# Kernel tuning notes

Measured on AMD Instinct MI355X. Metric: run time of the kernel, lower is better.

Reference implementation:

```python
import jax, jax.numpy as jnp
import numpy as np

NUM_CLASSES = 80
IOU_THR = 0.5
SCORE_THR = 0.25
MAX_BBOXES = 100
NEG = -1e9  # sentinel for suppressed scores


def setup_inputs() -> dict:
    key = jax.random.key(0)
    ks = jax.random.split(key, 9)
    B = 8
    def head(i, g):
        return (jax.random.uniform(ks[3*i], (B, g, g, 3, 4), dtype=jnp.float32),
                jax.random.uniform(ks[3*i+1], (B, g, g, 3, 1), dtype=jnp.float32),
                jax.random.normal(ks[3*i+2], (B, g, g, 3, NUM_CLASSES), dtype=jnp.float32))
    b20, p20, c20 = head(0, 20)
    b40, p40, c40 = head(1, 40)
    b80, p80, c80 = head(2, 80)
    return {"bbox20": b20, "p20": p20, "c20": c20,
            "bbox40": b40, "p40": p40, "c40": c40,
            "bbox80": b80, "p80": p80, "c80": c80}


def _iou_one_vs_all(box, boxes):
    # box: (4,) [y1,x1,y2,x2]; boxes: (N,4)
    y1, x1, y2, x2 = box[0], box[1], box[2], box[3]
    Y1, X1, Y2, X2 = boxes[:, 0], boxes[:, 1], boxes[:, 2], boxes[:, 3]
    ih = jnp.maximum(jnp.minimum(y2, Y2) - jnp.maximum(y1, Y1), 0.0)
    iw = jnp.maximum(jnp.minimum(x2, X2) - jnp.maximum(x1, X1), 0.0)
    inter = ih * iw
    union = (y2 - y1) * (x2 - x1) + (Y2 - Y1) * (X2 - X1) - inter
    return jnp.where(union > 0, inter / union, 0.0)


def _nms_single(boxes, scores):
    # boxes (N,4), scores (N,) -> greedy class-agnostic NMS, up to MAX_BBOXES
    sc0 = jnp.where(scores > SCORE_THR, scores, NEG)

    def body(sc, _):
        idx = jnp.argmax(sc)
        s = sc[idx]
        valid = s > NEG * 0.5
        box = boxes[idx]
        iou = _iou_one_vs_all(box, boxes)
        sc = jnp.where(iou > IOU_THR, NEG, sc)
        sc = sc.at[idx].set(NEG)
        ob = jnp.where(valid, jnp.clip(box, 0.0, 1.0), 0.0)  # clip_boxes=True default
        os = jnp.where(valid, s, 0.0)
        return sc, (ob, os, valid)

    _, (b, s, v) = jax.lax.scan(body, sc0, None, length=MAX_BBOXES)
    return b, s, jnp.sum(v.astype(jnp.int32))


def _forward(bbox20, p20, c20, bbox40, p40, c40, bbox80, p80, c80):
    B = bbox20.shape[0]
    bbox = jnp.concatenate([x.reshape(B, -1, 4) for x in (bbox20, bbox40, bbox80)], axis=1)
    p = jnp.concatenate([x.reshape(B, -1) for x in (p20, p40, p80)], axis=1)
    c = jnp.concatenate([x.reshape(B, -1, NUM_CLASSES) for x in (c20, c40, c80)], axis=1)
    cls = jnp.argmax(c, axis=-1).astype(jnp.float32)  # (B,N)
    score = p * cls  # quirky score = objectness * class index (faithful to source)
    b, s, valid = jax.vmap(_nms_single)(bbox, score)
    # classes output: scores had a single class dim in the TF op -> class index 0
    pred = jnp.concatenate([b, s[..., None], jnp.zeros_like(s)[..., None]], axis=-1)
    return pred, valid


def reference(bbox20, p20, c20, bbox40, p40, c40, bbox80, p80, c80):
    return _forward(bbox20, p20, c20, bbox40, p40, c40, bbox80, p80, c80)
```

## Files before the change

### kernel.cpp

```cpp
#include <hip/hip_runtime.h>
#include <hip/hip_bf16.h>

#define NUM_CLASSES 80
#define BATCH 8
#define N20 1200
#define N40 4800
#define N80 19200
#define NANCH 25200
#define NEGV  -1000000000.0f
#define SCORE_THR 0.25f
#define CAP 1024
#define RMAX 192
#define PKCAP 512
#define NHBIN 512
#define THR_LIST 64.0f

typedef unsigned long long ull;

__global__ __launch_bounds__(256) void score_kernel(
        const float* __restrict__ p20, const float* __restrict__ c20,
        const float* __restrict__ p40, const float* __restrict__ c40,
        const float* __restrict__ p80, const float* __restrict__ c80,
        float* __restrict__ scores, unsigned* __restrict__ cand_cnt,
        ull* __restrict__ cand_keys) {
    const int t = threadIdx.x;
    const int lane = t & 63;
    const int b = blockIdx.y;
    const int an = blockIdx.x * 256 + t;
    const bool valid_an = (an < NANCH);
    const int n = valid_an ? an : (NANCH - 1);

    const float *cp, *pp;
    if (n < N20) {
        cp = c20 + ((size_t)b * N20 + n) * NUM_CLASSES;
        pp = p20 + (size_t)b * N20 + n;
    } else if (n < N20 + N40) {
        int a = n - N20;
        cp = c40 + ((size_t)b * N40 + a) * NUM_CLASSES;
        pp = p40 + (size_t)b * N40 + a;
    } else {
        int a = n - N20 - N40;
        cp = c80 + ((size_t)b * N80 + a) * NUM_CLASSES;
        pp = p80 + (size_t)b * N80 + a;
    }

    const float4* c4 = (const float4*)cp;
    float p = *pp;
    float4 v[20];
#pragma unroll
    for (int k = 0; k < 20; k++) v[k] = c4[k];
    __builtin_amdgcn_sched_barrier(0);

    float best = -INFINITY;
    int bi = 0;
#pragma unroll
    for (int k = 0; k < 20; k++) {
        int basei = k * 4;
        if (v[k].x > best) { best = v[k].x; bi = basei; }
        if (v[k].y > best) { best = v[k].y; bi = basei + 1; }
        if (v[k].z > best) { best = v[k].z; bi = basei + 2; }
        if (v[k].w > best) { best = v[k].w; bi = basei + 3; }
    }

    float s = __fmul_rn(p, (float)bi);
    float sval = (s > SCORE_THR) ? s : NEGV;
    if (valid_an) scores[(size_t)b * NANCH + an] = sval;

    bool pred = valid_an && (s >= THR_LIST);
    ull mask = __ballot(pred);
    if (mask != 0ull) {
        int leader = (int)(__ffsll(mask) - 1);
        unsigned basep = 0;
        if (lane == leader) basep = atomicAdd(&cand_cnt[b], (unsigned)__popcll(mask));
        basep = __shfl(basep, leader);
        if (pred) {
            unsigned pos = basep + (unsigned)__popcll(mask & ((1ull << lane) - 1));
            if (pos < (unsigned)CAP)
                cand_keys[(size_t)b * CAP + pos] =
                    ((ull)__float_as_uint(s) << 32)
                  | (ull)(0xFFFFFFFFu - (unsigned)an);
        }
    }
}

__device__ __forceinline__ bool iou_gt(const float4 A, float areaA, const float4 Bx, float areaB) {
    float ih = fmaxf(__fsub_rn(fminf(A.z, Bx.z), fmaxf(A.x, Bx.x)), 0.0f);
    float iw = fmaxf(__fsub_rn(fminf(A.w, Bx.w), fmaxf(A.y, Bx.y)), 0.0f);
    float inter = __fmul_rn(ih, iw);
    float uni = __fsub_rn(__fadd_rn(areaA, areaB), inter);
    if (!(uni > 0.0f)) return false;
    return __fdiv_rn(inter, uni) > 0.5f;
}

__device__ __forceinline__ float4 load_box(int b, int n,
        const float* b20, const float* b40, const float* b80) {
    if (n < N20)       return ((const float4*)b20)[(size_t)b * N20 + n];
    if (n < N20 + N40) return ((const float4*)b40)[(size_t)b * N40 + (n - N20)];
    return ((const float4*)b80)[(size_t)b * N80 + (n - N20 - N40)];
}

__device__ __forceinline__ float box_area(const float4 B) {
    return __fmul_rn(__fsub_rn(B.z, B.x), __fsub_rn(B.w, B.y));
}

__global__ __launch_bounds__(1024) void nms_kernel(
        const float* __restrict__ scores_g,
        const unsigned* __restrict__ cand_cnt,
        const ull* __restrict__ cand_keys,
        const float* __restrict__ b20, const float* __restrict__ b40,
        const float* __restrict__ b80, float* __restrict__ out) {
    __shared__ ull skeys[CAP];
    __shared__ ull pk[PKCAP];
    __shared__ unsigned hist[NHBIN];
    __shared__ ull srt_key[RMAX];
    __shared__ int prt[PKCAP][5];
    __shared__ float4 bboxC[4][RMAX + 1];
    __shared__ ull M[RMAX][4];
    __shared__ ull red[1024];
    __shared__ int sh_V, sh_T;
    __shared__ unsigned sh_pcnt;

    const int t = threadIdx.x;
    const int lane = t & 63;
    const int b = blockIdx.x;

    const unsigned cnt_raw = cand_cnt[b];
    const bool use_list = (cnt_raw <= (unsigned)CAP);
    const int cnt = use_list ? (int)cnt_raw : 0;
    const int nR = min(cnt, RMAX);
    const unsigned need = (unsigned)nR;

    ull kmy = 0ull;
    float4 bmy = make_float4(0.f, 0.f, 0.f, 0.f);
    int mybin = 0;
    if (t < cnt) {
        kmy = cand_keys[(size_t)b * CAP + t];
        skeys[t] = kmy;
        bmy = load_box(b, (int)(0xFFFFFFFFu - (unsigned)(kmy & 0xFFFFFFFFull)),
                       b20, b40, b80);
        unsigned sb = (unsigned)(kmy >> 32);
        mybin = min((int)((sb - 0x42800000u) >> 12), NHBIN - 1);
    }
    if (t < NHBIN) hist[t] = 0u;
    if (t == 0) { sh_V = 0; sh_pcnt = 0u; }
    __syncthreads();

    if (t < cnt) atomicAdd(&hist[mybin], 1u);
    __syncthreads();

    if (t < 64) {
        unsigned h[8], sfx[8];
        const int basei = t * 8;
#pragma unroll
        for (int k = 0; k < 8; k++) h[k] = hist[basei + k];
        unsigned run = 0;
#pragma unroll
        for (int k = 7; k >= 0; k--) { run += h[k]; sfx[k] = run; }
        unsigned s = run;
#pragma unroll
        for (int d = 1; d < 64; d <<= 1) {
            unsigned vv = __shfl_down(s, d);
            if (t + d < 64) s += vv;
        }
        const unsigned above = s - run;
        int bestb = -1;
#pragma unroll
        for (int k = 0; k < 8; k++)
            if (sfx[k] + above >= need) bestb = basei + k;
#pragma unroll
        for (int d = 32; d > 0; d >>= 1) {
            int o = __shfl_down(bestb, d);
            if (t + d < 64) bestb = max(bestb, o);
        }
        if (t == 0) sh_T = max(bestb, 0);
    }
    __syncthreads();

    const bool part = (t < cnt) && (mybin >= sh_T);
    unsigned mypos = 0xFFFFFFFFu;
    {
        ull mask = __ballot(part);
        if (mask != 0ull) {
            int leader = (int)(__ffsll(mask) - 1);
            unsigned basep = 0;
            if (lane == leader) basep = atomicAdd(&sh_pcnt, (unsigned)__popcll(mask));
            basep = __shfl(basep, leader);
            if (part) {
                mypos = basep + (unsigned)__popcll(mask & ((1ull << lane) - 1));
                if (mypos < (unsigned)PKCAP) pk[mypos] = kmy;
            }
        }
    }
    __syncthreads();

    const int m = (int)sh_pcnt;
    const bool fastrank = (m <= PKCAP);

    if (fastrank) {
        const int q = t >> 8, u = t & 255;
        const ull kA = (u < m) ? pk[u] : 0ull;
        const ull kB = (u + 256 < m) ? pk[u + 256] : 0ull;
        const int Q = (m + 3) >> 2;
        const int j0 = q * Q, j1 = min(m, j0 + Q);
        int rA = 0, rB = 0;
#pragma unroll 8
        for (int j = j0; j < j1; j++) {
            ull kj = pk[j];
            rA += (kj > kA) ? 1 : 0;
            rB += (kj > kB) ? 1 : 0;
        }
        prt[u][q] = rA;
        if (u + 256 < PKCAP) prt[u + 256][q] = rB;
        __syncthreads();
        if (part && mypos < (unsigned)PKCAP) {
            int r = prt[mypos][0] + prt[mypos][1] + prt[mypos][2] + prt[mypos][3];
            if (r < RMAX) {
                srt_key[r] = kmy;
#pragma unroll
                for (int c = 0; c < 4; c++) bboxC[c][r] = bmy;
            }
        }
        __syncthreads();
    } else {
        const bool hasA = (t < 512) && (t < cnt);
        const bool hasB = (t < 512) && (t + 512 < cnt);
        ull kA = hasA ? skeys[t] : 0ull;
        ull kB = hasB ? skeys[t + 512] : 0ull;
        int rA = 0, rB = 0;
        if (t < 512) {
#pragma unroll 8
            for (int j = 0; j < cnt; j++) {
                ull kj = skeys[j];
                rA += (kj > kA) ? 1 : 0;
                rB += (kj > kB) ? 1 : 0;
            }
        }
        if (hasA && rA < RMAX) srt_key[rA] = kA;
        if (hasB && rB < RMAX) srt_key[rB] = kB;
        __syncthreads();
        if (t < nR) {
            ull k = srt_key[t];
            float4 B = load_box(b, (int)(0xFFFFFFFFu - (unsigned)(k & 0xFFFFFFFFull)),
                                b20, b40, b80);
#pragma unroll
            for (int c = 0; c < 4; c++) bboxC[c][t] = B;
        }
        __syncthreads();
    }

    {
        const int row = t >> 2, cw = t & 3;
        if (row < RMAX) {
            ull w = 0ull;
            if (row < nR && cw < 3 && cw * 64 < row) {
                const float4 B = bboxC[cw][row];
                const float aB = box_area(B);
                const int jmax = min(64, row - cw * 64);
                const float4* src = &bboxC[cw][cw * 64];
                for (int j = 0; j < jmax; j++) {
                    const float4 C = src[j];
                    w |= ((ull)iou_gt(C, box_area(C), B, aB)) << j;
                }
            }
            M[row][cw] = w;
        }
    }
    __syncthreads();

    int v = 0;
    if (t < 64) {
        ull A0 = 0, A1 = 0, A2 = 0;
        for (int rg = 0; rg < 3 && v < 100; rg++) {
            const int rr = rg * 64 + t;
            const bool valid = (rr < nR);
            ull w0 = 0, w1 = 0, w2 = 0;
            if (valid) { w0 = M[rr][0]; w1 = M[rr][1]; w2 = M[rr][2]; }
            const ull mw = (rg == 0) ? w0 : (rg == 1) ? w1 : w2;
            const bool supE = !valid ||
                (((w0 & A0) | (w1 & A1) | (w2 & A2)) != 0ull);
            ull alive = __ballot(!supE);
            while (alive != 0ull && v < 100) {
                int c = (int)(__ffsll(alive) - 1);
                ull supc = __ballot((bool)((mw >> c) & 1ull));
                alive &= ~(supc | (1ull << c));
                if (rg == 0) A0 |= 1ull << c;
                else if (rg == 1) A1 |= 1ull << c;
                else A2 |= 1ull << c;
                if (t == c) {
                    const float4 B = bboxC[0][rr];
                    float* rowp = out + ((size_t)b * 100 + v) * 6;
                    rowp[0] = fminf(fmaxf(B.x, 0.f), 1.f);
                    rowp[1] = fminf(fmaxf(B.y, 0.f), 1.f);
                    rowp[2] = fminf(fmaxf(B.z, 0.f), 1.f);
                    rowp[3] = fminf(fmaxf(B.w, 0.f), 1.f);
                    rowp[4] = __uint_as_float((unsigned)(srt_key[rr] >> 32));
                    rowp[5] = 0.f;
                }
                v++;
            }
        }
        if (t == 0) sh_V = v;
    }
    __syncthreads();

    const bool need_fb = (!use_list) || (sh_V < 100 && cnt > nR);
    if (need_fb) {
        float* scb = (float*)scores_g + (size_t)b * NANCH;
        int v2 = 0;
        for (int k = 0; k < 100; k++) {
            ull bestk = 0ull;
            for (int i = t; i < NANCH; i += 1024) {
                float sv = scb[i];
                unsigned u = __float_as_uint(sv);
                u ^= (u & 0x80000000u) ? 0xFFFFFFFFu : 0x80000000u;
                ull key = ((ull)u << 32) | (ull)(0xFFFFFFFFu - (unsigned)i);
                if (key > bestk) bestk = key;
            }
            red[t] = bestk;
            __syncthreads();
            for (int ss = 512; ss > 0; ss >>= 1) {
                if (t < ss && red[t + ss] > red[t]) red[t] = red[t + ss];
                __syncthreads();
            }
            ull bk = red[0];
            __syncthreads();
            unsigned u = (unsigned)(bk >> 32);
            u ^= (u & 0x80000000u) ? 0x80000000u : 0xFFFFFFFFu;
            float s = __uint_as_float(u);
            int idx = (int)(0xFFFFFFFFu - (unsigned)(bk & 0xFFFFFFFFull));
            if (!(s > NEGV * 0.5f)) break;
            float4 B = load_box(b, idx, b20, b40, b80);
            float aB = box_area(B);
            for (int i = t; i < NANCH; i += 1024) {
                float sv = scb[i];
                if (sv > NEGV * 0.5f) {
                    float4 C = load_box(b, i, b20, b40, b80);
                    if (iou_gt(B, aB, C, box_area(C))) scb[i] = NEGV;
                }
            }
            if (t == 0) {
                scb[idx] = NEGV;
                float* rowp = out + ((size_t)b * 100 + k) * 6;
                rowp[0] = fminf(fmaxf(B.x, 0.f), 1.f);
                rowp[1] = fminf(fmaxf(B.y, 0.f), 1.f);
                rowp[2] = fminf(fmaxf(B.z, 0.f), 1.f);
                rowp[3] = fminf(fmaxf(B.w, 0.f), 1.f);
                rowp[4] = s;
                rowp[5] = 0.f;
            }
            v2++;
            __syncthreads();
        }
        __syncthreads();
        if (t == 0) sh_V = v2;
        __syncthreads();
    }

    const int V = sh_V;
    for (int i = V * 6 + t; i < 600; i += 1024) out[(size_t)b * 600 + i] = 0.f;
    if (t == 0) out[4800 + b] = (float)V;
}

extern "C" void kernel_launch(void* const* d_in, const int* in_sizes, int n_in,
                              void* d_out, int out_size, void* d_ws, size_t ws_size,
                              hipStream_t stream) {
    const float* b20 = (const float*)d_in[0];
    const float* p20 = (const float*)d_in[1];
    const float* c20 = (const float*)d_in[2];
    const float* b40 = (const float*)d_in[3];
    const float* p40 = (const float*)d_in[4];
    const float* c40 = (const float*)d_in[5];
    const float* b80 = (const float*)d_in[6];
    const float* p80 = (const float*)d_in[7];
    const float* c80 = (const float*)d_in[8];

    float*    scores   = (float*)d_ws;
    unsigned* cand_cnt = (unsigned*)((char*)d_ws + 806400);
    ull*      cand_keys = (ull*)((char*)d_ws + 806464);

    hipMemsetAsync(cand_cnt, 0, BATCH * sizeof(unsigned), stream);

    dim3 sgrid((NANCH + 255) / 256, BATCH);
    score_kernel<<<sgrid, 256, 0, stream>>>(
        p20, c20, p40, c40, p80, c80, scores, cand_cnt, cand_keys);

    nms_kernel<<<BATCH, 1024, 0, stream>>>(
        scores, cand_cnt, cand_keys, b20, b40, b80, (float*)d_out);
}
```

Measured before the change: 164.8 us.

## Fuse score and NMS kernels with per-batch completion counters

Merges the scoring kernel and the NMS kernel into a single launch. The last 8 blocks spin on a per-batch done counter until all 99 scoring blocks for their batch finish, which removes one kernel launch boundary. The NMS part is reworked for 256 threads: it uses finer histogram bins, single-pass rank counting with box loads folded in, and a single box copy in shared memory instead of four. The risks are deadlock if the NMS blocks get scheduled before the scoring blocks and occupy the CUs, and slower NMS and fallback phases from using fewer threads.

Result: slower. 199.7 us (+21.2%).

```diff
diff --git a/kernel.cpp b/kernel.cpp
--- a/kernel.cpp
+++ b/kernel.cpp
@@ -12,76 +12,11 @@
 #define CAP 1024
 #define RMAX 192
 #define PKCAP 512
-#define NHBIN 512
+#define NHBIN 1024
 #define THR_LIST 64.0f
+#define NPB 99
 
 typedef unsigned long long ull;
-
-__global__ __launch_bounds__(256) void score_kernel(
-        const float* __restrict__ p20, const float* __restrict__ c20,
-        const float* __restrict__ p40, const float* __restrict__ c40,
-        const float* __restrict__ p80, const float* __restrict__ c80,
-        float* __restrict__ scores, unsigned* __restrict__ cand_cnt,
-        ull* __restrict__ cand_keys) {
-    const int t = threadIdx.x;
-    const int lane = t & 63;
-    const int b = blockIdx.y;
-    const int an = blockIdx.x * 256 + t;
-    const bool valid_an = (an < NANCH);
-    const int n = valid_an ? an : (NANCH - 1);
-
-    const float *cp, *pp;
-    if (n < N20) {
-        cp = c20 + ((size_t)b * N20 + n) * NUM_CLASSES;
-        pp = p20 + (size_t)b * N20 + n;
-    } else if (n < N20 + N40) {
-        int a = n - N20;
-        cp = c40 + ((size_t)b * N40 + a) * NUM_CLASSES;
-        pp = p40 + (size_t)b * N40 + a;
-    } else {
-        int a = n - N20 - N40;
-        cp = c80 + ((size_t)b * N80 + a) * NUM_CLASSES;
-        pp = p80 + (size_t)b * N80 + a;
-    }
-
-    const float4* c4 = (const float4*)cp;
-    float p = *pp;
-    float4 v[20];
-#pragma unroll
-    for (int k = 0; k < 20; k++) v[k] = c4[k];
-    __builtin_amdgcn_sched_barrier(0);
-
-    float best = -INFINITY;
-    int bi = 0;
-#pragma unroll
-    for (int k = 0; k < 20; k++) {
-        int basei = k * 4;
-        if (v[k].x > best) { best = v[k].x; bi = basei; }
-        if (v[k].y > best) { best = v[k].y; bi = basei + 1; }
-        if (v[k].z > best) { best = v[k].z; bi = basei + 2; }
-        if (v[k].w > best) { best = v[k].w; bi = basei + 3; }
-    }
-
-    float s = __fmul_rn(p, (float)bi);
-    float sval = (s > SCORE_THR) ? s : NEGV;
-    if (valid_an) scores[(size_t)b * NANCH + an] = sval;
-
-    bool pred = valid_an && (s >= THR_LIST);
-    ull mask = __ballot(pred);
-    if (mask != 0ull) {
-        int leader = (int)(__ffsll(mask) - 1);
-        unsigned basep = 0;
-        if (lane == leader) basep = atomicAdd(&cand_cnt[b], (unsigned)__popcll(mask));
-        basep = __shfl(basep, leader);
-        if (pred) {
-            unsigned pos = basep + (unsigned)__popcll(mask & ((1ull << lane) - 1));
-            if (pos < (unsigned)CAP)
-                cand_keys[(size_t)b * CAP + pos] =
-                    ((ull)__float_as_uint(s) << 32)
-                  | (ull)(0xFFFFFFFFu - (unsigned)an);
-        }
-    }
-}
 
 __device__ __forceinline__ bool iou_gt(const float4 A, float areaA, const float4 Bx, float areaB) {
     float ih = fmaxf(__fsub_rn(fminf(A.z, Bx.z), fmaxf(A.x, Bx.x)), 0.0f);
@@ -103,59 +38,139 @@
     return __fmul_rn(__fsub_rn(B.z, B.x), __fsub_rn(B.w, B.y));
 }
 
-__global__ __launch_bounds__(1024) void nms_kernel(
-        const float* __restrict__ scores_g,
-        const unsigned* __restrict__ cand_cnt,
-        const ull* __restrict__ cand_keys,
-        const float* __restrict__ b20, const float* __restrict__ b40,
-        const float* __restrict__ b80, float* __restrict__ out) {
+__device__ __forceinline__ int key_idx(ull k) {
+    return (int)(0xFFFFFFFFu - (unsigned)(k & 0xFFFFFFFFull));
+}
+
+__global__ __launch_bounds__(256) void fused_kernel(
+        const float* __restrict__ b20, const float* __restrict__ p20, const float* __restrict__ c20,
+        const float* __restrict__ b40, const float* __restrict__ p40, const float* __restrict__ c40,
+        const float* __restrict__ b80, const float* __restrict__ p80, const float* __restrict__ c80,
+        float* __restrict__ scores, unsigned* __restrict__ cand_cnt,
+        unsigned* __restrict__ done_cnt, ull* __restrict__ cand_keys,
+        float* __restrict__ out) {
     __shared__ ull skeys[CAP];
     __shared__ ull pk[PKCAP];
     __shared__ unsigned hist[NHBIN];
     __shared__ ull srt_key[RMAX];
-    __shared__ int prt[PKCAP][5];
-    __shared__ float4 bboxC[4][RMAX + 1];
-    __shared__ ull M[RMAX][4];
-    __shared__ ull red[1024];
+    __shared__ float4 bbox[RMAX];
+    __shared__ ull M[RMAX][3];
+    __shared__ ull red[256];
     __shared__ int sh_V, sh_T;
     __shared__ unsigned sh_pcnt;
 
     const int t = threadIdx.x;
     const int lane = t & 63;
-    const int b = blockIdx.x;
-
-    const unsigned cnt_raw = cand_cnt[b];
+    const int blk = blockIdx.x;
+
+    if (blk < BATCH * NPB) {
+        const int b = blk / NPB;
+        const int r = blk - b * NPB;
+        const int an = r * 256 + t;
+        const bool valid_an = (an < NANCH);
+        const int n = valid_an ? an : (NANCH - 1);
+
+        const float *cp, *pp;
+        if (n < N20) {
+            cp = c20 + ((size_t)b * N20 + n) * NUM_CLASSES;
+            pp = p20 + (size_t)b * N20 + n;
+        } else if (n < N20 + N40) {
+            int a = n - N20;
+            cp = c40 + ((size_t)b * N40 + a) * NUM_CLASSES;
+            pp = p40 + (size_t)b * N40 + a;
+        } else {
+            int a = n - N20 - N40;
+            cp = c80 + ((size_t)b * N80 + a) * NUM_CLASSES;
+            pp = p80 + (size_t)b * N80 + a;
+        }
+
+        const float4* c4 = (const float4*)cp;
+        float p = *pp;
+        float4 v[20];
+#pragma unroll
+        for (int k = 0; k < 20; k++) v[k] = c4[k];
+        __builtin_amdgcn_sched_barrier(0);
+
+        float best = -INFINITY;
+        int bi = 0;
+#pragma unroll
+        for (int k = 0; k < 20; k++) {
+            int basei = k * 4;
+            if (v[k].x > best) { best = v[k].x; bi = basei; }
+            if (v[k].y > best) { best = v[k].y; bi = basei + 1; }
+            if (v[k].z > best) { best = v[k].z; bi = basei + 2; }
+            if (v[k].w > best) { best = v[k].w; bi = basei + 3; }
+        }
+
+        float s = __fmul_rn(p, (float)bi);
+        float sval = (s > SCORE_THR) ? s : NEGV;
+        if (valid_an) scores[(size_t)b * NANCH + an] = sval;
+
+        bool pred = valid_an && (s >= THR_LIST);
+        ull mask = __ballot(pred);
+        if (mask != 0ull) {
+            int leader = (int)(__ffsll(mask) - 1);
+            unsigned basep = 0;
+            if (lane == leader) basep = atomicAdd(&cand_cnt[b], (unsigned)__popcll(mask));
+            basep = __shfl(basep, leader);
+            if (pred) {
+                unsigned pos = basep + (unsigned)__popcll(mask & ((1ull << lane) - 1));
+                if (pos < (unsigned)CAP)
+                    cand_keys[(size_t)b * CAP + pos] =
+                        ((ull)__float_as_uint(s) << 32)
+                      | (ull)(0xFFFFFFFFu - (unsigned)an);
+            }
+        }
+        __syncthreads();
+        if (t == 0) { __threadfence(); atomicAdd(&done_cnt[b], 1u); }
+        return;
+    }
+
+    const int b = blk - BATCH * NPB;
+
+    if (t == 0) {
+        while (__hip_atomic_load(&done_cnt[b], __ATOMIC_RELAXED,
+                                 __HIP_MEMORY_SCOPE_AGENT) < (unsigned)NPB)
+            __builtin_amdgcn_s_sleep(16);
+        __threadfence();
+        sh_V = 0; sh_pcnt = 0u;
+    }
+    for (int i = t; i < NHBIN; i += 256) hist[i] = 0u;
+    __syncthreads();
+
+    const unsigned cnt_raw = __hip_atomic_load(&cand_cnt[b], __ATOMIC_RELAXED,
+                                               __HIP_MEMORY_SCOPE_AGENT);
     const bool use_list = (cnt_raw <= (unsigned)CAP);
     const int cnt = use_list ? (int)cnt_raw : 0;
     const int nR = min(cnt, RMAX);
     const unsigned need = (unsigned)nR;
 
-    ull kmy = 0ull;
-    float4 bmy = make_float4(0.f, 0.f, 0.f, 0.f);
-    int mybin = 0;
-    if (t < cnt) {
-        kmy = cand_keys[(size_t)b * CAP + t];
-        skeys[t] = kmy;
-        bmy = load_box(b, (int)(0xFFFFFFFFu - (unsigned)(kmy & 0xFFFFFFFFull)),
-                       b20, b40, b80);
-        unsigned sb = (unsigned)(kmy >> 32);
-        mybin = min((int)((sb - 0x42800000u) >> 12), NHBIN - 1);
-    }
-    if (t < NHBIN) hist[t] = 0u;
-    if (t == 0) { sh_V = 0; sh_pcnt = 0u; }
-    __syncthreads();
-
-    if (t < cnt) atomicAdd(&hist[mybin], 1u);
+    ull k4[4]; int bin4[4];
+#pragma unroll
+    for (int i = 0; i < 4; i++) {
+        const int c = t + i * 256;
+        k4[i] = 0ull; bin4[i] = -1;
+        if (c < cnt) {
+            ull k = cand_keys[(size_t)b * CAP + c];
+            k4[i] = k;
+            skeys[c] = k;
+            unsigned sb = (unsigned)(k >> 32);
+            bin4[i] = min((int)((sb - 0x42800000u) >> 13), NHBIN - 1);
+        }
+    }
+    __syncthreads();
+#pragma unroll
+    for (int i = 0; i < 4; i++) if (bin4[i] >= 0) atomicAdd(&hist[bin4[i]], 1u);
     __syncthreads();
 
     if (t < 64) {
-        unsigned h[8], sfx[8];
-        const int basei = t * 8;
-#pragma unroll
-        for (int k = 0; k < 8; k++) h[k] = hist[basei + k];
+        unsigned h[16], sfx[16];
+        const int basei = t * 16;
+#pragma unroll
+        for (int k = 0; k < 16; k++) h[k] = hist[basei + k];
         unsigned run = 0;
 #pragma unroll
-        for (int k = 7; k >= 0; k--) { run += h[k]; sfx[k] = run; }
+        for (int k = 15; k >= 0; k--) { run += h[k]; sfx[k] = run; }
         unsigned s = run;
 #pragma unroll
         for (int d = 1; d < 64; d <<= 1) {
@@ -165,7 +180,7 @@
         const unsigned above = s - run;
         int bestb = -1;
 #pragma unroll
-        for (int k = 0; k < 8; k++)
+        for (int k = 0; k < 16; k++)
             if (sfx[k] + above >= need) bestb = basei + k;
 #pragma unroll
         for (int d = 32; d > 0; d >>= 1) {
@@ -175,10 +190,11 @@
         if (t == 0) sh_T = max(bestb, 0);
     }
     __syncthreads();
-
-    const bool part = (t < cnt) && (mybin >= sh_T);
-    unsigned mypos = 0xFFFFFFFFu;
-    {
+    const int T = sh_T;
+
+#pragma unroll
+    for (int i = 0; i < 4; i++) {
+        bool part = (bin4[i] >= T);
         ull mask = __ballot(part);
         if (mask != 0ull) {
             int leader = (int)(__ffsll(mask) - 1);
@@ -186,77 +202,57 @@
             if (lane == leader) basep = atomicAdd(&sh_pcnt, (unsigned)__popcll(mask));
             basep = __shfl(basep, leader);
             if (part) {
-                mypos = basep + (unsigned)__popcll(mask & ((1ull << lane) - 1));
-                if (mypos < (unsigned)PKCAP) pk[mypos] = kmy;
-            }
-        }
-    }
-    __syncthreads();
-
+                unsigned pos = basep + (unsigned)__popcll(mask & ((1ull << lane) - 1));
+                if (pos < (unsigned)PKCAP) pk[pos] = k4[i];
+            }
+        }
+    }
+    __syncthreads();
     const int m = (int)sh_pcnt;
-    const bool fastrank = (m <= PKCAP);
-
-    if (fastrank) {
-        const int q = t >> 8, u = t & 255;
-        const ull kA = (u < m) ? pk[u] : 0ull;
-        const ull kB = (u + 256 < m) ? pk[u + 256] : 0ull;
-        const int Q = (m + 3) >> 2;
-        const int j0 = q * Q, j1 = min(m, j0 + Q);
+
+    if (m <= PKCAP) {
+        ull kA = 0ull, kB = 0ull;
+        float4 bA = make_float4(0.f,0.f,0.f,0.f), bB = bA;
+        const bool hasA = (t < m), hasB = (t + 256 < m);
+        if (hasA) { kA = pk[t];        bA = load_box(b, key_idx(kA), b20, b40, b80); }
+        if (hasB) { kB = pk[t + 256];  bB = load_box(b, key_idx(kB), b20, b40, b80); }
         int rA = 0, rB = 0;
 #pragma unroll 8
-        for (int j = j0; j < j1; j++) {
+        for (int j = 0; j < m; j++) {
             ull kj = pk[j];
             rA += (kj > kA) ? 1 : 0;
             rB += (kj > kB) ? 1 : 0;
         }
-        prt[u][q] = rA;
-        if (u + 256 < PKCAP) prt[u + 256][q] = rB;
-        __syncthreads();
-        if (part && mypos < (unsigned)PKCAP) {
-            int r = prt[mypos][0] + prt[mypos][1] + prt[mypos][2] + prt[mypos][3];
-            if (r < RMAX) {
-                srt_key[r] = kmy;
-#pragma unroll
-                for (int c = 0; c < 4; c++) bboxC[c][r] = bmy;
-            }
-        }
+        if (hasA && rA < RMAX) { srt_key[rA] = kA; bbox[rA] = bA; }
+        if (hasB && rB < RMAX) { srt_key[rB] = kB; bbox[rB] = bB; }
         __syncthreads();
     } else {
-        const bool hasA = (t < 512) && (t < cnt);
-        const bool hasB = (t < 512) && (t + 512 < cnt);
-        ull kA = hasA ? skeys[t] : 0ull;
-        ull kB = hasB ? skeys[t + 512] : 0ull;
-        int rA = 0, rB = 0;
-        if (t < 512) {
-#pragma unroll 8
-            for (int j = 0; j < cnt; j++) {
-                ull kj = skeys[j];
-                rA += (kj > kA) ? 1 : 0;
-                rB += (kj > kB) ? 1 : 0;
-            }
-        }
-        if (hasA && rA < RMAX) srt_key[rA] = kA;
-        if (hasB && rB < RMAX) srt_key[rB] = kB;
-        __syncthreads();
-        if (t < nR) {
-            ull k = srt_key[t];
-            float4 B = load_box(b, (int)(0xFFFFFFFFu - (unsigned)(k & 0xFFFFFFFFull)),
-                                b20, b40, b80);
-#pragma unroll
-            for (int c = 0; c < 4; c++) bboxC[c][t] = B;
-        }
-        __syncthreads();
-    }
-
-    {
-        const int row = t >> 2, cw = t & 3;
-        if (row < RMAX) {
+        int r4[4] = {0, 0, 0, 0};
+        for (int j = 0; j < cnt; j++) {
+            ull kj = skeys[j];
+#pragma unroll
+            for (int i = 0; i < 4; i++) r4[i] += (kj > k4[i]) ? 1 : 0;
+        }
+#pragma unroll
+        for (int i = 0; i < 4; i++) {
+            const int c = t + i * 256;
+            if (c < cnt && r4[i] < RMAX) srt_key[r4[i]] = k4[i];
+        }
+        __syncthreads();
+        if (t < nR) bbox[t] = load_box(b, key_idx(srt_key[t]), b20, b40, b80);
+        __syncthreads();
+    }
+
+#pragma unroll
+    for (int cw = 0; cw < 3; cw++) {
+        if (t < RMAX) {
+            const int row = t;
             ull w = 0ull;
-            if (row < nR && cw < 3 && cw * 64 < row) {
-                const float4 B = bboxC[cw][row];
+            if (row < nR && cw * 64 < row) {
+                const float4 B = bbox[row];
                 const float aB = box_area(B);
                 const int jmax = min(64, row - cw * 64);
-                const float4* src = &bboxC[cw][cw * 64];
+                const float4* src = &bbox[cw * 64];
                 for (int j = 0; j < jmax; j++) {
                     const float4 C = src[j];
                     w |= ((ull)iou_gt(C, box_area(C), B, aB)) << j;
@@ -287,7 +283,7 @@
                 else if (rg == 1) A1 |= 1ull << c;
                 else A2 |= 1ull << c;
                 if (t == c) {
-                    const float4 B = bboxC[0][rr];
+                    const float4 B = bbox[rr];
                     float* rowp = out + ((size_t)b * 100 + v) * 6;
                     rowp[0] = fminf(fmaxf(B.x, 0.f), 1.f);
                     rowp[1] = fminf(fmaxf(B.y, 0.f), 1.f);
@@ -305,11 +301,11 @@
 
     const bool need_fb = (!use_list) || (sh_V < 100 && cnt > nR);
     if (need_fb) {
-        float* scb = (float*)scores_g + (size_t)b * NANCH;
+        float* scb = scores + (size_t)b * NANCH;
         int v2 = 0;
         for (int k = 0; k < 100; k++) {
             ull bestk = 0ull;
-            for (int i = t; i < NANCH; i += 1024) {
+            for (int i = t; i < NANCH; i += 256) {
                 float sv = scb[i];
                 unsigned u = __float_as_uint(sv);
                 u ^= (u & 0x80000000u) ? 0xFFFFFFFFu : 0x80000000u;
@@ -318,7 +314,7 @@
             }
             red[t] = bestk;
             __syncthreads();
-            for (int ss = 512; ss > 0; ss >>= 1) {
+            for (int ss = 128; ss > 0; ss >>= 1) {
                 if (t < ss && red[t + ss] > red[t]) red[t] = red[t + ss];
                 __syncthreads();
             }
@@ -331,7 +327,7 @@
             if (!(s > NEGV * 0.5f)) break;
             float4 B = load_box(b, idx, b20, b40, b80);
             float aB = box_area(B);
-            for (int i = t; i < NANCH; i += 1024) {
+            for (int i = t; i < NANCH; i += 256) {
                 float sv = scb[i];
                 if (sv > NEGV * 0.5f) {
                     float4 C = load_box(b, i, b20, b40, b80);
@@ -357,7 +353,7 @@
     }
 
     const int V = sh_V;
-    for (int i = V * 6 + t; i < 600; i += 1024) out[(size_t)b * 600 + i] = 0.f;
+    for (int i = V * 6 + t; i < 600; i += 256) out[(size_t)b * 600 + i] = 0.f;
     if (t == 0) out[4800 + b] = (float)V;
 }
 
@@ -376,14 +372,12 @@
 
     float*    scores   = (float*)d_ws;
     unsigned* cand_cnt = (unsigned*)((char*)d_ws + 806400);
+    unsigned* done_cnt = cand_cnt + BATCH;
     ull*      cand_keys = (ull*)((char*)d_ws + 806464);
 
-    hipMemsetAsync(cand_cnt, 0, BATCH * sizeof(unsigned), stream);
-
-    dim3 sgrid((NANCH + 255) / 256, BATCH);
-    score_kernel<<<sgrid, 256, 0, stream>>>(
-        p20, c20, p40, c40, p80, c80, scores, cand_cnt, cand_keys);
-
-    nms_kernel<<<BATCH, 1024, 0, stream>>>(
-        scores, cand_cnt, cand_keys, b20, b40, b80, (float*)d_out);
-}
+    hipMemsetAsync(cand_cnt, 0, 2 * BATCH * sizeof(unsigned), stream);
+
+    fused_kernel<<<BATCH * NPB + BATCH, 256, 0, stream>>>(
+        b20, p20, c20, b40, p40, c40, b80, p80, c80,
+        scores, cand_cnt, done_cnt, cand_keys, (float*)d_out);
+}
```

## Move candidate compaction into NMS kernel and drop memset launch

Applied to the files above, without the earlier changes.

The score kernel no longer does global atomics to build the candidate list. The NMS block now rescans its batch's score array with float4 loads, compacting candidates into shared memory and building the histogram in the same pass. This removes the hipMemsetAsync launch and the global atomics, but only 8 blocks now read the scores again. It also doubles CAP and the histogram bins, drops the duplicated bbox copies, and adds an occupancy hint to the score kernel.

New measurement: 152.9 us. 7.2% less time.

```diff
diff --git a/kernel.cpp b/kernel.cpp
--- a/kernel.cpp
+++ b/kernel.cpp
@@ -9,22 +9,20 @@
 #define NANCH 25200
 #define NEGV  -1000000000.0f
 #define SCORE_THR 0.25f
-#define CAP 1024
+#define CAP 2048
 #define RMAX 192
 #define PKCAP 512
-#define NHBIN 512
+#define NHBIN 1024
 #define THR_LIST 64.0f
 
 typedef unsigned long long ull;
 
-__global__ __launch_bounds__(256) void score_kernel(
+__global__ __launch_bounds__(256, 3) void score_kernel(
         const float* __restrict__ p20, const float* __restrict__ c20,
         const float* __restrict__ p40, const float* __restrict__ c40,
         const float* __restrict__ p80, const float* __restrict__ c80,
-        float* __restrict__ scores, unsigned* __restrict__ cand_cnt,
-        ull* __restrict__ cand_keys) {
+        float* __restrict__ scores) {
     const int t = threadIdx.x;
-    const int lane = t & 63;
     const int b = blockIdx.y;
     const int an = blockIdx.x * 256 + t;
     const bool valid_an = (an < NANCH);
@@ -65,22 +63,6 @@
     float s = __fmul_rn(p, (float)bi);
     float sval = (s > SCORE_THR) ? s : NEGV;
     if (valid_an) scores[(size_t)b * NANCH + an] = sval;
-
-    bool pred = valid_an && (s >= THR_LIST);
-    ull mask = __ballot(pred);
-    if (mask != 0ull) {
-        int leader = (int)(__ffsll(mask) - 1);
-        unsigned basep = 0;
-        if (lane == leader) basep = atomicAdd(&cand_cnt[b], (unsigned)__popcll(mask));
-        basep = __shfl(basep, leader);
-        if (pred) {
-            unsigned pos = basep + (unsigned)__popcll(mask & ((1ull << lane) - 1));
-            if (pos < (unsigned)CAP)
-                cand_keys[(size_t)b * CAP + pos] =
-                    ((ull)__float_as_uint(s) << 32)
-                  | (ull)(0xFFFFFFFFu - (unsigned)an);
-        }
-    }
 }
 
 __device__ __forceinline__ bool iou_gt(const float4 A, float areaA, const float4 Bx, float areaB) {
@@ -103,209 +85,224 @@
     return __fmul_rn(__fsub_rn(B.z, B.x), __fsub_rn(B.w, B.y));
 }
 
+__device__ __forceinline__ int key_idx(ull k) {
+    return (int)(0xFFFFFFFFu - (unsigned)(k & 0xFFFFFFFFull));
+}
+
 __global__ __launch_bounds__(1024) void nms_kernel(
-        const float* __restrict__ scores_g,
-        const unsigned* __restrict__ cand_cnt,
-        const ull* __restrict__ cand_keys,
+        float* __restrict__ scores,
         const float* __restrict__ b20, const float* __restrict__ b40,
         const float* __restrict__ b80, float* __restrict__ out) {
     __shared__ ull skeys[CAP];
     __shared__ ull pk[PKCAP];
     __shared__ unsigned hist[NHBIN];
+    __shared__ int prt[PKCAP][5];
     __shared__ ull srt_key[RMAX];
-    __shared__ int prt[PKCAP][5];
-    __shared__ float4 bboxC[4][RMAX + 1];
-    __shared__ ull M[RMAX][4];
+    __shared__ float4 bbox[RMAX];
+    __shared__ ull M[RMAX][3];
     __shared__ ull red[1024];
     __shared__ int sh_V, sh_T;
-    __shared__ unsigned sh_pcnt;
+    __shared__ unsigned sh_cnt, sh_pcnt;
 
     const int t = threadIdx.x;
     const int lane = t & 63;
     const int b = blockIdx.x;
 
-    const unsigned cnt_raw = cand_cnt[b];
-    const bool use_list = (cnt_raw <= (unsigned)CAP);
-    const int cnt = use_list ? (int)cnt_raw : 0;
-    const int nR = min(cnt, RMAX);
+    hist[t] = 0u;
+    if (t == 0) { sh_V = 0; sh_cnt = 0u; sh_pcnt = 0u; }
+    __syncthreads();
+
+    const float4* sc4 = (const float4*)(scores + (size_t)b * NANCH);
+#pragma unroll
+    for (int it = 0; it < 7; it++) {
+        const int i = t + it * 1024;
+        const bool in = (i < NANCH / 4);
+        float4 s4 = in ? sc4[i] : make_float4(NEGV, NEGV, NEGV, NEGV);
+        const float sv[4] = {s4.x, s4.y, s4.z, s4.w};
+#pragma unroll
+        for (int c = 0; c < 4; c++) {
+            const bool pred = in && (sv[c] >= THR_LIST);
+            ull mask = __ballot(pred);
+            if (mask != 0ull) {
+                int leader = (int)(__ffsll(mask) - 1);
+                unsigned basep = 0;
+                if (lane == leader) basep = atomicAdd(&sh_cnt, (unsigned)__popcll(mask));
+                basep = __shfl(basep, leader);
+                if (pred) {
+                    const unsigned sb = __float_as_uint(sv[c]);
+                    const unsigned an = (unsigned)(i * 4 + c);
+                    unsigned pos = basep + (unsigned)__popcll(mask & ((1ull << lane) - 1));
+                    if (pos < (unsigned)CAP)
+                        skeys[pos] = ((ull)sb << 32) | (ull)(0xFFFFFFFFu - an);
+                    atomicAdd(&hist[min((int)((sb - 0x42800000u) >> 13), NHBIN - 1)], 1u);
+                }
+            }
+        }
+    }
+    __syncthreads();
+
+    const int cnt = (int)sh_cnt;
+    const bool use_list = (cnt <= CAP);
+    const int nR = use_list ? min(cnt, RMAX) : 0;
     const unsigned need = (unsigned)nR;
 
-    ull kmy = 0ull;
-    float4 bmy = make_float4(0.f, 0.f, 0.f, 0.f);
-    int mybin = 0;
-    if (t < cnt) {
-        kmy = cand_keys[(size_t)b * CAP + t];
-        skeys[t] = kmy;
-        bmy = load_box(b, (int)(0xFFFFFFFFu - (unsigned)(kmy & 0xFFFFFFFFull)),
-                       b20, b40, b80);
-        unsigned sb = (unsigned)(kmy >> 32);
-        mybin = min((int)((sb - 0x42800000u) >> 12), NHBIN - 1);
-    }
-    if (t < NHBIN) hist[t] = 0u;
-    if (t == 0) { sh_V = 0; sh_pcnt = 0u; }
-    __syncthreads();
-
-    if (t < cnt) atomicAdd(&hist[mybin], 1u);
-    __syncthreads();
-
-    if (t < 64) {
-        unsigned h[8], sfx[8];
-        const int basei = t * 8;
-#pragma unroll
-        for (int k = 0; k < 8; k++) h[k] = hist[basei + k];
-        unsigned run = 0;
-#pragma unroll
-        for (int k = 7; k >= 0; k--) { run += h[k]; sfx[k] = run; }
-        unsigned s = run;
-#pragma unroll
-        for (int d = 1; d < 64; d <<= 1) {
-            unsigned vv = __shfl_down(s, d);
-            if (t + d < 64) s += vv;
-        }
-        const unsigned above = s - run;
-        int bestb = -1;
-#pragma unroll
-        for (int k = 0; k < 8; k++)
-            if (sfx[k] + above >= need) bestb = basei + k;
-#pragma unroll
-        for (int d = 32; d > 0; d >>= 1) {
-            int o = __shfl_down(bestb, d);
-            if (t + d < 64) bestb = max(bestb, o);
-        }
-        if (t == 0) sh_T = max(bestb, 0);
-    }
-    __syncthreads();
-
-    const bool part = (t < cnt) && (mybin >= sh_T);
-    unsigned mypos = 0xFFFFFFFFu;
-    {
-        ull mask = __ballot(part);
-        if (mask != 0ull) {
-            int leader = (int)(__ffsll(mask) - 1);
-            unsigned basep = 0;
-            if (lane == leader) basep = atomicAdd(&sh_pcnt, (unsigned)__popcll(mask));
-            basep = __shfl(basep, leader);
-            if (part) {
-                mypos = basep + (unsigned)__popcll(mask & ((1ull << lane) - 1));
-                if (mypos < (unsigned)PKCAP) pk[mypos] = kmy;
-            }
-        }
-    }
-    __syncthreads();
-
-    const int m = (int)sh_pcnt;
-    const bool fastrank = (m <= PKCAP);
-
-    if (fastrank) {
-        const int q = t >> 8, u = t & 255;
-        const ull kA = (u < m) ? pk[u] : 0ull;
-        const ull kB = (u + 256 < m) ? pk[u + 256] : 0ull;
-        const int Q = (m + 3) >> 2;
-        const int j0 = q * Q, j1 = min(m, j0 + Q);
-        int rA = 0, rB = 0;
+    if (use_list) {
+        if (t < 64) {
+            unsigned h[16], sfx[16];
+            const int basei = t * 16;
+#pragma unroll
+            for (int k = 0; k < 16; k++) h[k] = hist[basei + k];
+            unsigned run = 0;
+#pragma unroll
+            for (int k = 15; k >= 0; k--) { run += h[k]; sfx[k] = run; }
+            unsigned s = run;
+#pragma unroll
+            for (int d = 1; d < 64; d <<= 1) {
+                unsigned vv = __shfl_down(s, d);
+                if (t + d < 64) s += vv;
+            }
+            const unsigned above = s - run;
+            int bestb = -1;
+#pragma unroll
+            for (int k = 0; k < 16; k++)
+                if (sfx[k] + above >= need) bestb = basei + k;
+#pragma unroll
+            for (int d = 32; d > 0; d >>= 1) {
+                int o = __shfl_down(bestb, d);
+                if (t + d < 64) bestb = max(bestb, o);
+            }
+            if (t == 0) sh_T = max(bestb, 0);
+        }
+        __syncthreads();
+        const int T = sh_T;
+
+#pragma unroll
+        for (int h = 0; h < 2; h++) {
+            const int c = t + h * 1024;
+            bool part = false;
+            ull k = 0ull;
+            if (c < cnt) {
+                k = skeys[c];
+                int bin = min((int)(((unsigned)(k >> 32) - 0x42800000u) >> 13), NHBIN - 1);
+                part = (bin >= T);
+            }
+            ull mask = __ballot(part);
+            if (mask != 0ull) {
+                int leader = (int)(__ffsll(mask) - 1);
+                unsigned basep = 0;
+                if (lane == leader) basep = atomicAdd(&sh_pcnt, (unsigned)__popcll(mask));
+                basep = __shfl(basep, leader);
+                if (part) {
+                    unsigned pos = basep + (unsigned)__popcll(mask & ((1ull << lane) - 1));
+                    if (pos < (unsigned)PKCAP) pk[pos] = k;
+                }
+            }
+        }
+        __syncthreads();
+        const int m = (int)sh_pcnt;
+
+        if (m <= PKCAP) {
+            ull kmy = 0ull;
+            float4 bmy = make_float4(0.f, 0.f, 0.f, 0.f);
+            if (t < m) {
+                kmy = pk[t];
+                bmy = load_box(b, key_idx(kmy), b20, b40, b80);
+            }
+            const int q = t >> 8, u = t & 255;
+            const ull kA = (u < m) ? pk[u] : 0ull;
+            const ull kB = (u + 256 < m) ? pk[u + 256] : 0ull;
+            const int Q = (m + 3) >> 2;
+            const int j0 = q * Q, j1 = min(m, j0 + Q);
+            int rA = 0, rB = 0;
 #pragma unroll 8
-        for (int j = j0; j < j1; j++) {
-            ull kj = pk[j];
-            rA += (kj > kA) ? 1 : 0;
-            rB += (kj > kB) ? 1 : 0;
-        }
-        prt[u][q] = rA;
-        if (u + 256 < PKCAP) prt[u + 256][q] = rB;
-        __syncthreads();
-        if (part && mypos < (unsigned)PKCAP) {
-            int r = prt[mypos][0] + prt[mypos][1] + prt[mypos][2] + prt[mypos][3];
-            if (r < RMAX) {
-                srt_key[r] = kmy;
-#pragma unroll
-                for (int c = 0; c < 4; c++) bboxC[c][r] = bmy;
-            }
-        }
-        __syncthreads();
-    } else {
-        const bool hasA = (t < 512) && (t < cnt);
-        const bool hasB = (t < 512) && (t + 512 < cnt);
-        ull kA = hasA ? skeys[t] : 0ull;
-        ull kB = hasB ? skeys[t + 512] : 0ull;
-        int rA = 0, rB = 0;
-        if (t < 512) {
-#pragma unroll 8
+            for (int j = j0; j < j1; j++) {
+                ull kj = pk[j];
+                rA += (kj > kA) ? 1 : 0;
+                rB += (kj > kB) ? 1 : 0;
+            }
+            prt[u][q] = rA;
+            prt[u + 256][q] = rB;
+            __syncthreads();
+            if (t < m) {
+                int r = prt[t][0] + prt[t][1] + prt[t][2] + prt[t][3];
+                if (r < RMAX) { srt_key[r] = kmy; bbox[r] = bmy; }
+            }
+            __syncthreads();
+        } else {
+            ull kA = (t < cnt) ? skeys[t] : 0ull;
+            ull kB = (t + 1024 < cnt) ? skeys[t + 1024] : 0ull;
+            int rA = 0, rB = 0;
             for (int j = 0; j < cnt; j++) {
                 ull kj = skeys[j];
                 rA += (kj > kA) ? 1 : 0;
                 rB += (kj > kB) ? 1 : 0;
             }
-        }
-        if (hasA && rA < RMAX) srt_key[rA] = kA;
-        if (hasB && rB < RMAX) srt_key[rB] = kB;
-        __syncthreads();
-        if (t < nR) {
-            ull k = srt_key[t];
-            float4 B = load_box(b, (int)(0xFFFFFFFFu - (unsigned)(k & 0xFFFFFFFFull)),
-                                b20, b40, b80);
-#pragma unroll
-            for (int c = 0; c < 4; c++) bboxC[c][t] = B;
-        }
-        __syncthreads();
-    }
-
-    {
-        const int row = t >> 2, cw = t & 3;
-        if (row < RMAX) {
-            ull w = 0ull;
-            if (row < nR && cw < 3 && cw * 64 < row) {
-                const float4 B = bboxC[cw][row];
-                const float aB = box_area(B);
-                const int jmax = min(64, row - cw * 64);
-                const float4* src = &bboxC[cw][cw * 64];
-                for (int j = 0; j < jmax; j++) {
-                    const float4 C = src[j];
-                    w |= ((ull)iou_gt(C, box_area(C), B, aB)) << j;
-                }
-            }
-            M[row][cw] = w;
-        }
-    }
-    __syncthreads();
-
-    int v = 0;
-    if (t < 64) {
-        ull A0 = 0, A1 = 0, A2 = 0;
-        for (int rg = 0; rg < 3 && v < 100; rg++) {
-            const int rr = rg * 64 + t;
-            const bool valid = (rr < nR);
-            ull w0 = 0, w1 = 0, w2 = 0;
-            if (valid) { w0 = M[rr][0]; w1 = M[rr][1]; w2 = M[rr][2]; }
-            const ull mw = (rg == 0) ? w0 : (rg == 1) ? w1 : w2;
-            const bool supE = !valid ||
-                (((w0 & A0) | (w1 & A1) | (w2 & A2)) != 0ull);
-            ull alive = __ballot(!supE);
-            while (alive != 0ull && v < 100) {
-                int c = (int)(__ffsll(alive) - 1);
-                ull supc = __ballot((bool)((mw >> c) & 1ull));
-                alive &= ~(supc | (1ull << c));
-                if (rg == 0) A0 |= 1ull << c;
-                else if (rg == 1) A1 |= 1ull << c;
-                else A2 |= 1ull << c;
-                if (t == c) {
-                    const float4 B = bboxC[0][rr];
-                    float* rowp = out + ((size_t)b * 100 + v) * 6;
-                    rowp[0] = fminf(fmaxf(B.x, 0.f), 1.f);
-                    rowp[1] = fminf(fmaxf(B.y, 0.f), 1.f);
-                    rowp[2] = fminf(fmaxf(B.z, 0.f), 1.f);
-                    rowp[3] = fminf(fmaxf(B.w, 0.f), 1.f);
-                    rowp[4] = __uint_as_float((unsigned)(srt_key[rr] >> 32));
-                    rowp[5] = 0.f;
-                }
-                v++;
-            }
-        }
-        if (t == 0) sh_V = v;
-    }
-    __syncthreads();
+            if (t < cnt && rA < RMAX) srt_key[rA] = kA;
+            if (t + 1024 < cnt && rB < RMAX) srt_key[rB] = kB;
+            __syncthreads();
+            if (t < nR) bbox[t] = load_box(b, key_idx(srt_key[t]), b20, b40, b80);
+            __syncthreads();
+        }
+
+        {
+            const int row = t >> 2, cw = t & 3;
+            if (row < RMAX && cw < 3) {
+                ull w = 0ull;
+                if (row < nR && cw * 64 < row) {
+                    const float4 B = bbox[row];
+                    const float aB = box_area(B);
+                    const int jmax = min(64, row - cw * 64);
+                    const float4* src = &bbox[cw * 64];
+                    for (int j = 0; j < jmax; j++) {
+                        const float4 C = src[j];
+                        w |= ((ull)iou_gt(C, box_area(C), B, aB)) << j;
+                    }
+                }
+                M[row][cw] = w;
+            }
+        }
+        __syncthreads();
+
+        int v = 0;
+        if (t < 64) {
+            ull A0 = 0, A1 = 0, A2 = 0;
+            for (int rg = 0; rg < 3 && v < 100; rg++) {
+                const int rr = rg * 64 + t;
+                const bool valid = (rr < nR);
+                ull w0 = 0, w1 = 0, w2 = 0;
+                if (valid) { w0 = M[rr][0]; w1 = M[rr][1]; w2 = M[rr][2]; }
+                const ull mw = (rg == 0) ? w0 : (rg == 1) ? w1 : w2;
+                const bool supE = !valid ||
+                    (((w0 & A0) | (w1 & A1) | (w2 & A2)) != 0ull);
+                ull alive = __ballot(!supE);
+                while (alive != 0ull && v < 100) {
+                    int c = (int)(__ffsll(alive) - 1);
+                    ull supc = __ballot((bool)((mw >> c) & 1ull));
+                    alive &= ~(supc | (1ull << c));
+                    if (rg == 0) A0 |= 1ull << c;
+                    else if (rg == 1) A1 |= 1ull << c;
+                    else A2 |= 1ull << c;
+                    if (t == c) {
+                        const float4 B = bbox[rr];
+                        float* rowp = out + ((size_t)b * 100 + v) * 6;
+                        rowp[0] = fminf(fmaxf(B.x, 0.f), 1.f);
+                        rowp[1] = fminf(fmaxf(B.y, 0.f), 1.f);
+                        rowp[2] = fminf(fmaxf(B.z, 0.f), 1.f);
+                        rowp[3] = fminf(fmaxf(B.w, 0.f), 1.f);
+                        rowp[4] = __uint_as_float((unsigned)(srt_key[rr] >> 32));
+                        rowp[5] = 0.f;
+                    }
+                    v++;
+                }
+            }
+            if (t == 0) sh_V = v;
+        }
+        __syncthreads();
+    }
 
     const bool need_fb = (!use_list) || (sh_V < 100 && cnt > nR);
     if (need_fb) {
-        float* scb = (float*)scores_g + (size_t)b * NANCH;
+        float* scb = scores + (size_t)b * NANCH;
         int v2 = 0;
         for (int k = 0; k < 100; k++) {
             ull bestk = 0ull;
@@ -374,16 +371,12 @@
     const float* p80 = (const float*)d_in[7];
     const float* c80 = (const float*)d_in[8];
 
-    float*    scores   = (float*)d_ws;
-    unsigned* cand_cnt = (unsigned*)((char*)d_ws + 806400);
-    ull*      cand_keys = (ull*)((char*)d_ws + 806464);
-
-    hipMemsetAsync(cand_cnt, 0, BATCH * sizeof(unsigned), stream);
+    float* scores = (float*)d_ws;
 
     dim3 sgrid((NANCH + 255) / 256, BATCH);
     score_kernel<<<sgrid, 256, 0, stream>>>(
-        p20, c20, p40, c40, p80, c80, scores, cand_cnt, cand_keys);
+        p20, c20, p40, c40, p80, c80, scores);
 
     nms_kernel<<<BATCH, 1024, 0, stream>>>(
-        scores, cand_cnt, cand_keys, b20, b40, b80, (float*)d_out);
-}
+        scores, b20, b40, b80, (float*)d_out);
+}
```
